# Optimization experiments

Hardware: AMD Instinct MI355X
Metric: run time of the kernel (lower is better)

Reference implementation:

```python
import jax, jax.numpy as jnp
import numpy as np

# ---- model constants (stand-ins for the Qiskit circuit / SparsePauliOp) ----
Q = 20           # qubits
L = 4            # ansatz layers: RY on every qubit, then ring of CZ
R = 24           # tensor-ring bond rank (init kwarg `rank`)
P = Q * L        # number of circuit parameters
CDT = jnp.complex64

_CZ = jnp.asarray(np.diag([1.0, 1.0, 1.0, -1.0]).reshape(2, 2, 2, 2), CDT)

# Observable H = 0.8*Z0 Z1 + 0.5*Z3 (Z/I-only -> 'efficient' expectation path)
_TERMS = [(0.8, (0, 1)), (0.5, (3,))]
_ZDIAG = jnp.asarray([1.0, -1.0], CDT)


def _init_cores():
    # |0...0> product state embedded in rank-R ring cores (identity bonds),
    # plus a tiny fixed perturbation so truncated-SVD singular values are
    # generic (keeps jax.vjp through SVD well-conditioned).
    rng = np.random.default_rng(0)
    cores = []
    for _ in range(Q):
        c = np.zeros((R, 2, R), np.complex64)
        c[:, 0, :] = np.eye(R, dtype=np.complex64)
        c = c + 1e-2 * (rng.standard_normal((R, 2, R))
                        + 1j * rng.standard_normal((R, 2, R))).astype(np.complex64)
        cores.append(jnp.asarray(c))
    return cores

_INIT_CORES = _init_cores()


def _apply_1q(core, U2):
    # core: (R, 2, R); U2: (2, 2) acting on the physical index
    return jnp.einsum('ts,asb->atb', U2, core)


def _apply_2q(ci, cj, U4):
    # merge neighboring ring cores, apply 4x4 gate, split via truncated SVD
    theta = jnp.einsum('asb,btc->astc', ci, cj)        # (R,2,2,R)
    theta = jnp.einsum('uvst,astc->auvc', U4, theta)   # gate on physical (s,t)
    M = theta.reshape(2 * R, 2 * R)
    Uu, s, Vh = jnp.linalg.svd(M, full_matrices=False)
    sr = jnp.sqrt(s[:R]).astype(CDT)                   # split sqrt(s) both ways
    ci_new = (Uu[:, :R] * sr[None, :]).reshape(R, 2, R)
    cj_new = (sr[:, None] * Vh[:R, :]).reshape(R, 2, R)
    return ci_new, cj_new


def _ring_ev(cores, zqubits):
    # <psi| (prod_i D_i) |psi> for diagonal D_i in {I, Z}; trace-closed ring.
    # Boundary M[p,q,b,r]: p/b = ket open/running bonds, q/r = bra bonds.
    eye = jnp.eye(R, dtype=CDT)
    M = jnp.einsum('ab,cd->acbd', eye, eye)            # (R,R,R,R)
    zset = set(zqubits)
    for i in range(Q):
        A = cores[i]
        Ad = A * _ZDIAG[None, :, None] if i in zset else A
        T = jnp.einsum('pqbr,bsc->pqrsc', M, Ad)       # contract ket bond, 2R^5
        M = jnp.einsum('pqrsc,rsd->pqcd', T, jnp.conj(A))  # bra bond + phys
    return jnp.einsum('pqpq->', M)                     # close the ring trace


def _forward(params):
    cores = list(_INIT_CORES)
    idx = 0
    for _ in range(L):
        for q in range(Q):
            half = params[idx] * 0.5
            idx += 1
            c, s = jnp.cos(half), jnp.sin(half)
            U2 = jnp.stack([jnp.stack([c, -s]), jnp.stack([s, c])]).astype(CDT)
            cores[q] = _apply_1q(cores[q], U2)
        for q in range(Q):                              # ring of CZ (wraps)
            j = (q + 1) % Q
            cores[q], cores[j] = _apply_2q(cores[q], cores[j], _CZ)
    norm = jnp.real(_ring_ev(cores, ()))
    ev = sum(c * jnp.real(_ring_ev(cores, zq)) for c, zq in _TERMS)
    return (ev / norm).astype(jnp.float32)


def setup_inputs() -> dict:
    key = jax.random.key(0)
    params = jax.random.normal(key, (P,), dtype=jnp.float32)
    return {"params": params}


def reference(params):
    return _forward(params)
```

## Files before the change

### kernel.cpp

```cpp
#include <hip/hip_runtime.h>
#include <cstdint>
#include <cmath>
#include <cstring>


#define RK 24
#define NQ 20
#define NLAY 4
#define NCOL 48
#define AS 49
#define NSWEEP 8
#define NTHR 384
#define CORE_ELEMS (RK * 2 * RK)
#define M4 (RK * RK * RK * RK)

namespace npyrng {

struct Pcg64 {
  unsigned __int128 state, inc;
  static inline unsigned __int128 mult() {
    return (((unsigned __int128)0x2360ED051FC65DA4ull) << 64) |
           0x4385DF649FCCF645ull;
  }
  inline void step() { state = state * mult() + inc; }
  inline uint64_t next64() {
    step();
    uint64_t hi = (uint64_t)(state >> 64), lo = (uint64_t)state;
    uint64_t v = hi ^ lo;
    unsigned r = (unsigned)(state >> 122);
    return (v >> r) | (v << ((64u - r) & 63u));
  }
  inline double nextDouble() {
    return (double)(next64() >> 11) * (1.0 / 9007199254740992.0);
  }
};

struct ZigTables {
  uint64_t ki[256];
  double wi[256], fi[256];
};

static void build_tables(ZigTables& T) {
  const double NR = 3.6541528853610088;
  const double PI = 3.14159265358979323846;
  double f = std::exp(-0.5 * NR * NR);
  double V = NR * f + std::sqrt(PI / 2.0) * std::erfc(NR / std::sqrt(2.0));
  const double m1 = 4503599627370496.0;
  double q = V / f;
  T.ki[0] = (uint64_t)((NR / q) * m1);
  T.ki[1] = 0;
  T.wi[0] = q / m1;
  T.wi[255] = NR / m1;
  T.fi[0] = 1.0;
  T.fi[255] = f;
  double tn = NR;
  for (int i = 254; i >= 1; --i) {
    double dn = std::sqrt(-2.0 * std::log(V / tn + std::exp(-0.5 * tn * tn)));
    T.ki[i + 1] = (uint64_t)((dn / tn) * m1);
    T.fi[i] = std::exp(-0.5 * dn * dn);
    T.wi[i] = dn / m1;
    tn = dn;
  }
}

static double std_normal(Pcg64& g, const ZigTables& T) {
  const double NR = 3.6541528853610088;
  const double INV_NR = 0.27366123732975828;
  for (;;) {
    uint64_t r = g.next64();
    int idx = (int)(r & 0xff);
    r >>= 8;
    int sign = (int)(r & 1);
    uint64_t rabs = (r >> 1) & 0x000fffffffffffffull;
    double x = (double)rabs * T.wi[idx];
    if (sign) x = -x;
    if (rabs < T.ki[idx]) return x;
    if (idx == 0) {
      for (;;) {
        double xx = -INV_NR * std::log1p(-g.nextDouble());
        double yy = -std::log1p(-g.nextDouble());
        if (yy + yy > xx * xx)
          return ((rabs >> 8) & 1) ? -(NR + xx) : (NR + xx);
      }
    } else {
      if ((T.fi[idx - 1] - T.fi[idx]) * g.nextDouble() + T.fi[idx] <
          std::exp(-0.5 * x * x))
        return x;
    }
  }
}

static void seed_pcg64_numpy0(Pcg64& g) {
  const uint32_t INIT_A = 0x43b0d7e5u, MULT_A = 0x931e8875u;
  const uint32_t INIT_B = 0x8b51f9ddu, MULT_B = 0x58f38dedu;
  const uint32_t MIX_L = 0xca01f9ddu, MIX_R = 0x4973f715u;
  uint32_t pool[4];
  uint32_t hc = INIT_A;
  auto hashf = [&](uint32_t value) -> uint32_t {
    value ^= hc;
    hc *= MULT_A;
    value *= hc;
    value ^= value >> 16;
    return value;
  };
  auto mixf = [&](uint32_t x, uint32_t y) -> uint32_t {
    uint32_t r = x * MIX_L - y * MIX_R;
    r ^= r >> 16;
    return r;
  };
  uint32_t entropy0 = 0u;
  for (int i = 0; i < 4; ++i) pool[i] = hashf(i < 1 ? entropy0 : 0u);
  for (int s = 0; s < 4; ++s)
    for (int d = 0; d < 4; ++d)
      if (s != d) pool[d] = mixf(pool[d], hashf(pool[s]));
  uint32_t w[8];
  uint32_t hb = INIT_B;
  for (int i = 0; i < 8; ++i) {
    uint32_t dv = pool[i & 3];
    dv ^= hb;
    hb *= MULT_B;
    dv *= hb;
    dv ^= dv >> 16;
    w[i] = dv;
  }
  uint64_t v0 = (uint64_t)w[0] | ((uint64_t)w[1] << 32);
  uint64_t v1 = (uint64_t)w[2] | ((uint64_t)w[3] << 32);
  uint64_t v2 = (uint64_t)w[4] | ((uint64_t)w[5] << 32);
  uint64_t v3 = (uint64_t)w[6] | ((uint64_t)w[7] << 32);
  unsigned __int128 initstate = (((unsigned __int128)v0) << 64) | v1;
  unsigned __int128 initseq = (((unsigned __int128)v2) << 64) | v3;
  g.state = 0;
  g.inc = (initseq << 1) | 1;
  g.step();
  g.state += initstate;
  g.step();
}

}

static float h_cores[NQ * CORE_ELEMS * 2];

static void fill_host_cores() {
  npyrng::Pcg64 g;
  npyrng::seed_pcg64_numpy0(g);
  npyrng::ZigTables T;
  npyrng::build_tables(T);
  double re[CORE_ELEMS], im[CORE_ELEMS];
  for (int core = 0; core < NQ; ++core) {
    for (int t = 0; t < CORE_ELEMS; ++t) re[t] = npyrng::std_normal(g, T);
    for (int t = 0; t < CORE_ELEMS; ++t) im[t] = npyrng::std_normal(g, T);
    for (int o = 0; o < CORE_ELEMS; ++o) {
      int a = o / (2 * RK);
      int s = (o / RK) & 1;
      int b = o % RK;
      float baser = (s == 0 && a == b) ? 1.0f : 0.0f;
      float nr = (float)re[o], ni = (float)im[o];
      h_cores[(core * CORE_ELEMS + o) * 2 + 0] = baser + 0.01f * nr;
      h_cores[(core * CORE_ELEMS + o) * 2 + 1] = 0.01f * ni;
    }
  }
}

__device__ __forceinline__ float row_reduce16(float x) {
  int v;
  v = __builtin_amdgcn_update_dpp(0, __float_as_int(x), 0x128, 0xf, 0xf, false);
  x += __int_as_float(v);
  v = __builtin_amdgcn_update_dpp(0, __float_as_int(x), 0x124, 0xf, 0xf, false);
  x += __int_as_float(v);
  v = __builtin_amdgcn_update_dpp(0, __float_as_int(x), 0x122, 0xf, 0xf, false);
  x += __int_as_float(v);
  v = __builtin_amdgcn_update_dpp(0, __float_as_int(x), 0x121, 0xf, 0xf, false);
  x += __int_as_float(v);
  return x;
}

__global__ __launch_bounds__(NTHR) void evolve_kernel(
    const float* __restrict__ params, float2* __restrict__ cores) {
  __shared__ float2 A[NCOL * AS];
  __shared__ float2 S1[NCOL * AS];
  __shared__ float2 M0[NCOL * NCOL];
  __shared__ float n0[NCOL], n1[NCOL];
  __shared__ float sig2[NCOL];
  __shared__ int keepSrc[RK];
  __shared__ float csbuf[NQ * 2];
  __shared__ int sweepFlag;

  const int tid = threadIdx.x;
  const int team = tid >> 4;
  const int sub = tid & 15;

  const int tdst = (team == 0) ? 0 : ((team < 23) ? team + 1 : 47);
  const int bdst = (team == 0) ? 1 : (23 + team);
  const int tsrc = team;
  const int bsrc = 24 + team;

  if (tid == 0) sweepFlag = 0;

  for (int layer = 0; layer < NLAY; ++layer) {
    if (tid < NQ) {
      float half = 0.5f * params[layer * NQ + tid];
      csbuf[2 * tid] = cosf(half);
      csbuf[2 * tid + 1] = sinf(half);
    }
    __syncthreads();
    for (int o = tid; o < NQ * RK * RK; o += NTHR) {
      int qq = o / (RK * RK);
      int ab = o % (RK * RK);
      int a = ab / RK, b = ab % RK;
      float ch = csbuf[2 * qq], sh = csbuf[2 * qq + 1];
      float2* base = cores + qq * CORE_ELEMS;
      float2 c0 = base[(a * 2 + 0) * RK + b];
      float2 c1 = base[(a * 2 + 1) * RK + b];
      base[(a * 2 + 0) * RK + b] =
          make_float2(ch * c0.x - sh * c1.x, ch * c0.y - sh * c1.y);
      base[(a * 2 + 1) * RK + b] =
          make_float2(sh * c0.x + ch * c1.x, sh * c0.y + ch * c1.y);
    }
    __syncthreads();

    for (int qg = 0; qg < NQ; ++qg) {
      int jg = (qg + 1) % NQ;
      const float2* ci = cores + qg * CORE_ELEMS;
      const float2* cj = cores + jg * CORE_ELEMS;

      for (int o = tid; o < CORE_ELEMS; o += NTHR) {
        M0[o] = ci[o];
        M0[CORE_ELEMS + o] = cj[o];
      }
      __syncthreads();

      float2 mv[6];
      {
        int k = 0;
        for (int o = tid; o < NCOL * NCOL; o += NTHR, ++k) {
          int col = o / NCOL, row = o % NCOL;
          int a = row >> 1, s = row & 1;
          int t = col / RK, cc = col % RK;
          float accx = 0.f, accy = 0.f;
          for (int b = 0; b < RK; ++b) {
            float2 x = M0[(a * 2 + s) * RK + b];
            float2 y = M0[CORE_ELEMS + (b * 2 + t) * RK + cc];
            accx += x.x * y.x - x.y * y.y;
            accy += x.x * y.y + x.y * y.x;
          }
          if (s == 1 && t == 1) { accx = -accx; accy = -accy; }
          mv[k] = make_float2(accx, accy);
        }
      }
      __syncthreads();
      {
        int k = 0;
        for (int o = tid; o < NCOL * NCOL; o += NTHR, ++k) {
          int col = o / NCOL, row = o % NCOL;
          A[col * AS + row] = mv[k];
          M0[col * NCOL + row] = mv[k];
        }
      }
      __syncthreads();

      float2 t0 = A[tsrc * AS + sub], t1 = A[tsrc * AS + sub + 16],
             t2 = A[tsrc * AS + sub + 32];
      float2 b0 = A[bsrc * AS + sub], b1 = A[bsrc * AS + sub + 16],
             b2 = A[bsrc * AS + sub + 32];
      float nt = t0.x * t0.x + t0.y * t0.y + t1.x * t1.x + t1.y * t1.y +
                 t2.x * t2.x + t2.y * t2.y;
      float nb = b0.x * b0.x + b0.y * b0.y + b1.x * b1.x + b1.y * b1.y +
                 b2.x * b2.x + b2.y * b2.y;
      nt = row_reduce16(nt);
      nb = row_reduce16(nb);

      int rr = 0;
      for (int sw = 0; sw < NSWEEP; ++sw) {
        bool myActive = false;
        for (int r = 0; r < 47; ++r) {
          float pr = t0.x * b0.x + t0.y * b0.y + t1.x * b1.x + t1.y * b1.y +
                     t2.x * b2.x + t2.y * b2.y;
          float pi = t0.x * b0.y - t0.y * b0.x + t1.x * b1.y - t1.y * b1.x +
                     t2.x * b2.y - t2.y * b2.x;
          pr = row_reduce16(pr);
          pi = row_reduce16(pi);
          float m2 = pr * pr + pi * pi;
          myActive = myActive || (m2 > 1e-7f * nt * nb);
          if (m2 > 1e-30f && m2 > 1e-14f * nt * nb) {
            float inv_m = rsqrtf(m2);
            float zr = pr * inv_m, zi = pi * inv_m;
            float tau = (nt - nb) * 0.5f * inv_m;
            float tt = 1.f / (fabsf(tau) + sqrtf(1.f + tau * tau));
            if (tau < 0.f) tt = -tt;
            float cc_ = rsqrtf(1.f + tt * tt);
            float ss_ = tt * cc_;
#define ROT_PAIR(xp, xq)                                                     \
  {                                                                          \
    float zqr = zr * xq.x + zi * xq.y;                                       \
    float zqi = zr * xq.y - zi * xq.x;                                       \
    float zpr = zr * xp.x - zi * xp.y;                                       \
    float zpi = zr * xp.y + zi * xp.x;                                       \
    float2 npv = make_float2(cc_ * xp.x + ss_ * zqr, cc_ * xp.y + ss_ * zqi);\
    float2 nqv = make_float2(cc_ * xq.x - ss_ * zpr, cc_ * xq.y - ss_ * zpi);\
    xp = npv;                                                                \
    xq = nqv;                                                                \
  }
            ROT_PAIR(t0, b0);
            ROT_PAIR(t1, b1);
            ROT_PAIR(t2, b2);
#undef ROT_PAIR
            float mg = m2 * inv_m;
            float c2 = cc_ * cc_, s2 = ss_ * ss_;
            float cs2m = 2.f * cc_ * ss_ * mg;
            float ntn = c2 * nt + s2 * nb + cs2m;
            nb = s2 * nt + c2 * nb - cs2m;
            nt = ntn;
          }
          float2* wb = (rr & 1) ? A : S1;
          float* wn = (rr & 1) ? n0 : n1;
          wb[tdst * AS + sub] = t0;
          wb[tdst * AS + sub + 16] = t1;
          wb[tdst * AS + sub + 32] = t2;
          wb[bdst * AS + sub] = b0;
          wb[bdst * AS + sub + 16] = b1;
          wb[bdst * AS + sub + 32] = b2;
          if (sub == 0) {
            wn[tdst] = nt;
            wn[bdst] = nb;
          }
          __syncthreads();
          t0 = wb[tsrc * AS + sub];
          t1 = wb[tsrc * AS + sub + 16];
          t2 = wb[tsrc * AS + sub + 32];
          b0 = wb[bsrc * AS + sub];
          b1 = wb[bsrc * AS + sub + 16];
          b2 = wb[bsrc * AS + sub + 32];
          nt = wn[tsrc];
          nb = wn[bsrc];
          ++rr;
        }
        unsigned long long bal = __ballot(myActive);
        if ((tid & 63) == 0 && bal != 0ull) sweepFlag = 1;
        __syncthreads();
        int f = sweepFlag;
        __syncthreads();
        if (tid == 0) sweepFlag = 0;
        if (f == 0) break;
      }

      A[tsrc * AS + sub] = t0;
      A[tsrc * AS + sub + 16] = t1;
      A[tsrc * AS + sub + 32] = t2;
      A[bsrc * AS + sub] = b0;
      A[bsrc * AS + sub + 16] = b1;
      A[bsrc * AS + sub + 32] = b2;
      {
        float xt = t0.x * t0.x + t0.y * t0.y + t1.x * t1.x + t1.y * t1.y +
                   t2.x * t2.x + t2.y * t2.y;
        float xb = b0.x * b0.x + b0.y * b0.y + b1.x * b1.x + b1.y * b1.y +
                   b2.x * b2.x + b2.y * b2.y;
        xt = row_reduce16(xt);
        xb = row_reduce16(xb);
        if (sub == 0) {
          sig2[tsrc] = xt;
          sig2[bsrc] = xb;
        }
      }
      __syncthreads();

      if (tid < NCOL) {
        float mine = sig2[tid];
        int rk = 0;
        for (int kx = 0; kx < NCOL; ++kx) {
          float o = sig2[kx];
          if (o > mine || (o == mine && kx < tid)) ++rk;
        }
        if (rk < RK) keepSrc[rk] = tid;
      }
      __syncthreads();

      for (int o = tid; o < RK * NCOL; o += NTHR) {
        int bn = o / NCOL;
        int row = o % NCOL;
        int src = keepSrc[bn];
        float sg = sqrtf(sig2[src]);
        float su = rsqrtf(fmaxf(sg, 1e-30f));
        float2 x = A[src * AS + row];
        cores[qg * CORE_ELEMS + row * RK + bn] =
            make_float2(x.x * su, x.y * su);
      }
      for (int o = tid; o < RK * NCOL; o += NTHR) {
        int bn = o / NCOL;
        int col = o % NCOL;
        int src = keepSrc[bn];
        float s2 = fmaxf(sig2[src], 1e-30f);
        float scale = rsqrtf(s2) * rsqrtf(sqrtf(s2));
        float accx = 0.f, accy = 0.f;
        const float2* ac = &A[src * AS];
        const float2* mc = &M0[col * NCOL];
#pragma unroll 8
        for (int rx = 0; rx < NCOL; ++rx) {
          float2 u = ac[rx];
          float2 mm = mc[rx];
          accx += u.x * mm.x + u.y * mm.y;
          accy += u.x * mm.y - u.y * mm.x;
        }
        cores[jg * CORE_ELEMS + bn * (2 * RK) + col] =
            make_float2(accx * scale, accy * scale);
      }
      __syncthreads();
    }
  }
}

__global__ __launch_bounds__(256) void init_m_kernel(float2* __restrict__ mb) {
  int i = blockIdx.x * 256 + threadIdx.x;
  if (i >= M4) return;
  int r = i % RK;
  int b = (i / RK) % RK;
  int q = (i / (RK * RK)) % RK;
  int p = i / (RK * RK * RK);
  mb[i] = make_float2((p == b && q == r) ? 1.f : 0.f, 0.f);
}

__global__ __launch_bounds__(256) void ring_step_kernel(
    const float2* __restrict__ Min, float2* __restrict__ Mout,
    const float2* __restrict__ cores, int qubit, int zmask) {
  __shared__ float2 Msh[RK * RK];
  __shared__ float2 Ash[CORE_ELEMS];
  __shared__ float2 Tsh[RK * 2 * RK];
  const int pq = blockIdx.x;
  const float zs = ((zmask >> qubit) & 1) ? -1.f : 1.f;
  const float2* minpq = Min + (size_t)pq * (RK * RK);
  for (int o = threadIdx.x; o < RK * RK; o += 256) Msh[o] = minpq[o];
  const float2* Ac = cores + qubit * CORE_ELEMS;
  for (int o = threadIdx.x; o < CORE_ELEMS; o += 256) Ash[o] = Ac[o];
  __syncthreads();
  for (int o = threadIdx.x; o < RK * 2 * RK; o += 256) {
    int r = o / (2 * RK);
    int sc = o % (2 * RK);
    int s = sc / RK, c = sc % RK;
    float sgn = (s == 1) ? zs : 1.f;
    float accx = 0.f, accy = 0.f;
#pragma unroll 8
    for (int b = 0; b < RK; ++b) {
      float2 m = Msh[b * RK + r];
      float2 a = Ash[(b * 2 + s) * RK + c];
      accx += m.x * a.x - m.y * a.y;
      accy += m.x * a.y + m.y * a.x;
    }
    Tsh[o] = make_float2(accx * sgn, accy * sgn);
  }
  __syncthreads();
  float2* moutpq = Mout + (size_t)pq * (RK * RK);
  for (int o = threadIdx.x; o < RK * RK; o += 256) {
    int c = o / RK, d = o % RK;
    float accx = 0.f, accy = 0.f;
    for (int r = 0; r < RK; ++r)
#pragma unroll
      for (int s = 0; s < 2; ++s) {
        float2 t = Tsh[r * (2 * RK) + s * RK + c];
        float2 a = Ash[(r * 2 + s) * RK + d];
        accx += t.x * a.x + t.y * a.y;
        accy += t.y * a.x - t.x * a.y;
      }
    moutpq[o] = make_float2(accx, accy);
  }
}

__global__ __launch_bounds__(256) void trace_kernel(
    const float2* __restrict__ mb, float* __restrict__ dst) {
  __shared__ float sh[4];
  float tr = 0.f;
  for (int o = threadIdx.x; o < RK * RK; o += 256) {
    int p = o / RK, q = o % RK;
    tr += mb[(size_t)o * (RK * RK) + p * RK + q].x;
  }
  for (int d = 1; d < 64; d <<= 1) tr += __shfl_xor(tr, d);
  int wave = threadIdx.x >> 6, lane = threadIdx.x & 63;
  if (lane == 0) sh[wave] = tr;
  __syncthreads();
  if (threadIdx.x == 0) dst[0] = sh[0] + sh[1] + sh[2] + sh[3];
}

__global__ void final_kernel(const float* __restrict__ trs,
                             float* __restrict__ out) {
  if (threadIdx.x == 0)
    out[0] = (0.8f * trs[1] + 0.5f * trs[2]) / trs[0];
}

extern "C" void kernel_launch(void* const* d_in, const int* in_sizes, int n_in,
                              void* d_out, int out_size, void* d_ws,
                              size_t ws_size, hipStream_t stream) {
  const float* params = (const float*)d_in[0];
  float* out = (float*)d_out;
  char* ws = (char*)d_ws;

  const size_t CORES_BYTES = sizeof(h_cores);
  const size_t MB_BYTES = (size_t)M4 * sizeof(float2);
  float2* cores = (float2*)ws;
  float2* B0 = (float2*)(ws + CORES_BYTES);
  float2* B1 = (float2*)(ws + CORES_BYTES + MB_BYTES);
  float2* B2 = (float2*)(ws + CORES_BYTES + 2 * MB_BYTES);
  float* tr_ws = (float*)(ws + CORES_BYTES + 3 * MB_BYTES);

  fill_host_cores();
  hipMemcpyAsync(cores, h_cores, CORES_BYTES, hipMemcpyHostToDevice, stream);

  evolve_kernel<<<1, NTHR, 0, stream>>>(params, cores);

  init_m_kernel<<<(M4 + 255) / 256, 256, 0, stream>>>(B0);
  for (int qb = 4; qb < 20; ++qb) {
    const float2* src = ((qb - 4) & 1) ? B1 : B0;
    float2* dst = ((qb - 4) & 1) ? B0 : B1;
    ring_step_kernel<<<RK * RK, 256, 0, stream>>>(src, dst, cores, qb, 0);
  }
  for (int e = 0; e < 3; ++e) {
    int zm = (e == 0) ? 0 : (e == 1 ? 3 : 8);
    ring_step_kernel<<<RK * RK, 256, 0, stream>>>(B0, B1, cores, 0, zm);
    ring_step_kernel<<<RK * RK, 256, 0, stream>>>(B1, B2, cores, 1, zm);
    ring_step_kernel<<<RK * RK, 256, 0, stream>>>(B2, B1, cores, 2, zm);
    ring_step_kernel<<<RK * RK, 256, 0, stream>>>(B1, B2, cores, 3, zm);
    trace_kernel<<<1, 256, 0, stream>>>(B2, tr_ws + e);
  }
  final_kernel<<<1, 64, 0, stream>>>(tr_ws, out);
}
```

Measured before the change: 18.49 ms.

## Use 8-lane teams with packed float2 math in one-sided Jacobi SVD

The Jacobi SVD sweep now uses 8 lanes per column pair instead of 16, with only 192 active threads. Each lane holds six complex elements in split real/imag packed-float2 vectors so the compiler can emit packed FP32 ops. The DPP reduction is shortened to three steps, and the shared-memory ping-pong buffer switches to float4 layout. The sweep convergence threshold is also loosened from 1e-7 to 1e-5, which may cut sweeps at some cost in SVD accuracy.

Measured after the change: 17.76 ms. 1.04x faster.

```diff
diff --git a/kernel.cpp b/kernel.cpp
--- a/kernel.cpp
+++ b/kernel.cpp
@@ -9,10 +9,14 @@
 #define NLAY 4
 #define NCOL 48
 #define AS 49
+#define ASQ 25
 #define NSWEEP 8
 #define NTHR 384
+#define NACT 192
 #define CORE_ELEMS (RK * 2 * RK)
 #define M4 (RK * RK * RK * RK)
+
+typedef float v2f __attribute__((ext_vector_type(2)));
 
 namespace npyrng {
 
@@ -161,15 +165,13 @@
   }
 }
 
-__device__ __forceinline__ float row_reduce16(float x) {
+__device__ __forceinline__ float red8(float x) {
   int v;
-  v = __builtin_amdgcn_update_dpp(0, __float_as_int(x), 0x128, 0xf, 0xf, false);
+  v = __builtin_amdgcn_update_dpp(0, __float_as_int(x), 0xB1, 0xf, 0xf, false);
   x += __int_as_float(v);
-  v = __builtin_amdgcn_update_dpp(0, __float_as_int(x), 0x124, 0xf, 0xf, false);
+  v = __builtin_amdgcn_update_dpp(0, __float_as_int(x), 0x4E, 0xf, 0xf, false);
   x += __int_as_float(v);
-  v = __builtin_amdgcn_update_dpp(0, __float_as_int(x), 0x122, 0xf, 0xf, false);
-  x += __int_as_float(v);
-  v = __builtin_amdgcn_update_dpp(0, __float_as_int(x), 0x121, 0xf, 0xf, false);
+  v = __builtin_amdgcn_update_dpp(0, __float_as_int(x), 0x141, 0xf, 0xf, false);
   x += __int_as_float(v);
   return x;
 }
@@ -177,7 +179,8 @@
 __global__ __launch_bounds__(NTHR) void evolve_kernel(
     const float* __restrict__ params, float2* __restrict__ cores) {
   __shared__ float2 A[NCOL * AS];
-  __shared__ float2 S1[NCOL * AS];
+  __shared__ float4 A4[NCOL * ASQ];
+  __shared__ float4 S4[NCOL * ASQ];
   __shared__ float2 M0[NCOL * NCOL];
   __shared__ float n0[NCOL], n1[NCOL];
   __shared__ float sig2[NCOL];
@@ -186,15 +189,16 @@
   __shared__ int sweepFlag;
 
   const int tid = threadIdx.x;
-  const int team = tid >> 4;
-  const int sub = tid & 15;
+  const bool act = tid < NACT;
+  const int team = tid >> 3;
+  const int l8 = tid & 7;
 
   const int tdst = (team == 0) ? 0 : ((team < 23) ? team + 1 : 47);
   const int bdst = (team == 0) ? 1 : (23 + team);
-  const int tsrc = team;
-  const int bsrc = 24 + team;
+  const int tsrc = team, bsrc = 24 + team;
 
   if (tid == 0) sweepFlag = 0;
+  int rr = 0;
 
   for (int layer = 0; layer < NLAY; ++layer) {
     if (tid < NQ) {
@@ -258,83 +262,113 @@
       }
       __syncthreads();
 
-      float2 t0 = A[tsrc * AS + sub], t1 = A[tsrc * AS + sub + 16],
-             t2 = A[tsrc * AS + sub + 32];
-      float2 b0 = A[bsrc * AS + sub], b1 = A[bsrc * AS + sub + 16],
-             b2 = A[bsrc * AS + sub + 32];
-      float nt = t0.x * t0.x + t0.y * t0.y + t1.x * t1.x + t1.y * t1.y +
-                 t2.x * t2.x + t2.y * t2.y;
-      float nb = b0.x * b0.x + b0.y * b0.y + b1.x * b1.x + b1.y * b1.y +
-                 b2.x * b2.x + b2.y * b2.y;
-      nt = row_reduce16(nt);
-      nb = row_reduce16(nb);
-
-      int rr = 0;
+      v2f tR0 = {0, 0}, tR1 = {0, 0}, tR2 = {0, 0};
+      v2f tI0 = {0, 0}, tI1 = {0, 0}, tI2 = {0, 0};
+      v2f bR0 = {0, 0}, bR1 = {0, 0}, bR2 = {0, 0};
+      v2f bI0 = {0, 0}, bI1 = {0, 0}, bI2 = {0, 0};
+      float nt = 0.f, nb = 0.f;
+      if (act) {
+        const float2* cp = &A[tsrc * AS + 6 * l8];
+        float2 u0 = cp[0], u1 = cp[1], u2 = cp[2], u3 = cp[3], u4 = cp[4],
+               u5 = cp[5];
+        tR0 = (v2f){u0.x, u1.x}; tI0 = (v2f){u0.y, u1.y};
+        tR1 = (v2f){u2.x, u3.x}; tI1 = (v2f){u2.y, u3.y};
+        tR2 = (v2f){u4.x, u5.x}; tI2 = (v2f){u4.y, u5.y};
+        cp = &A[bsrc * AS + 6 * l8];
+        u0 = cp[0]; u1 = cp[1]; u2 = cp[2]; u3 = cp[3]; u4 = cp[4]; u5 = cp[5];
+        bR0 = (v2f){u0.x, u1.x}; bI0 = (v2f){u0.y, u1.y};
+        bR1 = (v2f){u2.x, u3.x}; bI1 = (v2f){u2.y, u3.y};
+        bR2 = (v2f){u4.x, u5.x}; bI2 = (v2f){u4.y, u5.y};
+        v2f Nt = tR0 * tR0 + tI0 * tI0 + tR1 * tR1 + tI1 * tI1 + tR2 * tR2 +
+                 tI2 * tI2;
+        v2f Nb = bR0 * bR0 + bI0 * bI0 + bR1 * bR1 + bI1 * bI1 + bR2 * bR2 +
+                 bI2 * bI2;
+        nt = red8(Nt.x + Nt.y);
+        nb = red8(Nb.x + Nb.y);
+      }
+      __syncthreads();
+
       for (int sw = 0; sw < NSWEEP; ++sw) {
         bool myActive = false;
         for (int r = 0; r < 47; ++r) {
-          float pr = t0.x * b0.x + t0.y * b0.y + t1.x * b1.x + t1.y * b1.y +
-                     t2.x * b2.x + t2.y * b2.y;
-          float pi = t0.x * b0.y - t0.y * b0.x + t1.x * b1.y - t1.y * b1.x +
-                     t2.x * b2.y - t2.y * b2.x;
-          pr = row_reduce16(pr);
-          pi = row_reduce16(pi);
-          float m2 = pr * pr + pi * pi;
-          myActive = myActive || (m2 > 1e-7f * nt * nb);
-          if (m2 > 1e-30f && m2 > 1e-14f * nt * nb) {
-            float inv_m = rsqrtf(m2);
-            float zr = pr * inv_m, zi = pi * inv_m;
-            float tau = (nt - nb) * 0.5f * inv_m;
-            float tt = 1.f / (fabsf(tau) + sqrtf(1.f + tau * tau));
-            if (tau < 0.f) tt = -tt;
-            float cc_ = rsqrtf(1.f + tt * tt);
-            float ss_ = tt * cc_;
-#define ROT_PAIR(xp, xq)                                                     \
-  {                                                                          \
-    float zqr = zr * xq.x + zi * xq.y;                                       \
-    float zqi = zr * xq.y - zi * xq.x;                                       \
-    float zpr = zr * xp.x - zi * xp.y;                                       \
-    float zpi = zr * xp.y + zi * xp.x;                                       \
-    float2 npv = make_float2(cc_ * xp.x + ss_ * zqr, cc_ * xp.y + ss_ * zqi);\
-    float2 nqv = make_float2(cc_ * xq.x - ss_ * zpr, cc_ * xq.y - ss_ * zpi);\
-    xp = npv;                                                                \
-    xq = nqv;                                                                \
-  }
-            ROT_PAIR(t0, b0);
-            ROT_PAIR(t1, b1);
-            ROT_PAIR(t2, b2);
-#undef ROT_PAIR
-            float mg = m2 * inv_m;
-            float c2 = cc_ * cc_, s2 = ss_ * ss_;
-            float cs2m = 2.f * cc_ * ss_ * mg;
-            float ntn = c2 * nt + s2 * nb + cs2m;
-            nb = s2 * nt + c2 * nb - cs2m;
-            nt = ntn;
-          }
-          float2* wb = (rr & 1) ? A : S1;
-          float* wn = (rr & 1) ? n0 : n1;
-          wb[tdst * AS + sub] = t0;
-          wb[tdst * AS + sub + 16] = t1;
-          wb[tdst * AS + sub + 32] = t2;
-          wb[bdst * AS + sub] = b0;
-          wb[bdst * AS + sub + 16] = b1;
-          wb[bdst * AS + sub + 32] = b2;
-          if (sub == 0) {
-            wn[tdst] = nt;
-            wn[bdst] = nb;
+          if (act) {
+            v2f Pr = tR0 * bR0 + tI0 * bI0;
+            Pr += tR1 * bR1 + tI1 * bI1;
+            Pr += tR2 * bR2 + tI2 * bI2;
+            v2f Pi = tR0 * bI0 - tI0 * bR0;
+            Pi += tR1 * bI1 - tI1 * bR1;
+            Pi += tR2 * bI2 - tI2 * bR2;
+            float pr = red8(Pr.x + Pr.y);
+            float pi = red8(Pi.x + Pi.y);
+            float m2 = pr * pr + pi * pi;
+            myActive = myActive || (m2 > 1e-5f * nt * nb);
+            if (m2 > 1e-30f && m2 > 1e-14f * nt * nb) {
+              float inv_m = rsqrtf(m2);
+              float zr = pr * inv_m, zi = pi * inv_m;
+              float tau = (nt - nb) * 0.5f * inv_m;
+              float tt = 1.f / (fabsf(tau) + sqrtf(1.f + tau * tau));
+              if (tau < 0.f) tt = -tt;
+              float cc_ = rsqrtf(1.f + tt * tt);
+              float ss_ = tt * cc_;
+              v2f zrv = {zr, zr}, ziv = {zi, zi};
+              v2f ccv = {cc_, cc_}, ssv = {ss_, ss_};
+#define ROTK(TR, TI, BR, BI)                                   \
+  {                                                            \
+    v2f zqR = zrv * BR + ziv * BI;                             \
+    v2f zqI = zrv * BI - ziv * BR;                             \
+    v2f zpR = zrv * TR - ziv * TI;                             \
+    v2f zpI = zrv * TI + ziv * TR;                             \
+    TR = ccv * TR + ssv * zqR;                                 \
+    TI = ccv * TI + ssv * zqI;                                 \
+    BR = ccv * BR - ssv * zpR;                                 \
+    BI = ccv * BI - ssv * zpI;                                 \
+  }
+              ROTK(tR0, tI0, bR0, bI0);
+              ROTK(tR1, tI1, bR1, bI1);
+              ROTK(tR2, tI2, bR2, bI2);
+#undef ROTK
+              float mg = m2 * inv_m;
+              float c2 = cc_ * cc_, s2 = ss_ * ss_;
+              float cs2m = 2.f * cc_ * ss_ * mg;
+              float ntn = c2 * nt + s2 * nb + cs2m;
+              nb = s2 * nt + c2 * nb - cs2m;
+              nt = ntn;
+            }
+            float4* wb = (rr & 1) ? A4 : S4;
+            float* wn = (rr & 1) ? n0 : n1;
+            int tb = tdst * ASQ + l8 * 3;
+            wb[tb + 0] = make_float4(tR0.x, tR0.y, tI0.x, tI0.y);
+            wb[tb + 1] = make_float4(tR1.x, tR1.y, tI1.x, tI1.y);
+            wb[tb + 2] = make_float4(tR2.x, tR2.y, tI2.x, tI2.y);
+            int bb = bdst * ASQ + l8 * 3;
+            wb[bb + 0] = make_float4(bR0.x, bR0.y, bI0.x, bI0.y);
+            wb[bb + 1] = make_float4(bR1.x, bR1.y, bI1.x, bI1.y);
+            wb[bb + 2] = make_float4(bR2.x, bR2.y, bI2.x, bI2.y);
+            if (l8 == 0) {
+              wn[tdst] = nt;
+              wn[bdst] = nb;
+            }
           }
           __syncthreads();
-          t0 = wb[tsrc * AS + sub];
-          t1 = wb[tsrc * AS + sub + 16];
-          t2 = wb[tsrc * AS + sub + 32];
-          b0 = wb[bsrc * AS + sub];
-          b1 = wb[bsrc * AS + sub + 16];
-          b2 = wb[bsrc * AS + sub + 32];
-          nt = wn[tsrc];
-          nb = wn[bsrc];
+          if (act) {
+            const float4* wb = (rr & 1) ? A4 : S4;
+            const float* wn = (rr & 1) ? n0 : n1;
+            int ts = tsrc * ASQ + l8 * 3;
+            float4 q0 = wb[ts + 0], q1 = wb[ts + 1], q2 = wb[ts + 2];
+            tR0 = (v2f){q0.x, q0.y}; tI0 = (v2f){q0.z, q0.w};
+            tR1 = (v2f){q1.x, q1.y}; tI1 = (v2f){q1.z, q1.w};
+            tR2 = (v2f){q2.x, q2.y}; tI2 = (v2f){q2.z, q2.w};
+            int bs = bsrc * ASQ + l8 * 3;
+            q0 = wb[bs + 0]; q1 = wb[bs + 1]; q2 = wb[bs + 2];
+            bR0 = (v2f){q0.x, q0.y}; bI0 = (v2f){q0.z, q0.w};
+            bR1 = (v2f){q1.x, q1.y}; bI1 = (v2f){q1.z, q1.w};
+            bR2 = (v2f){q2.x, q2.y}; bI2 = (v2f){q2.z, q2.w};
+            nt = wn[tsrc];
+            nb = wn[bsrc];
+          }
           ++rr;
         }
-        unsigned long long bal = __ballot(myActive);
+        unsigned long long bal = __ballot(act && myActive);
         if ((tid & 63) == 0 && bal != 0ull) sweepFlag = 1;
         __syncthreads();
         int f = sweepFlag;
@@ -343,20 +377,28 @@
         if (f == 0) break;
       }
 
-      A[tsrc * AS + sub] = t0;
-      A[tsrc * AS + sub + 16] = t1;
-      A[tsrc * AS + sub + 32] = t2;
-      A[bsrc * AS + sub] = b0;
-      A[bsrc * AS + sub + 16] = b1;
-      A[bsrc * AS + sub + 32] = b2;
-      {
-        float xt = t0.x * t0.x + t0.y * t0.y + t1.x * t1.x + t1.y * t1.y +
-                   t2.x * t2.x + t2.y * t2.y;
-        float xb = b0.x * b0.x + b0.y * b0.y + b1.x * b1.x + b1.y * b1.y +
-                   b2.x * b2.x + b2.y * b2.y;
-        xt = row_reduce16(xt);
-        xb = row_reduce16(xb);
-        if (sub == 0) {
+      if (act) {
+        float2* cp = &A[tsrc * AS + 6 * l8];
+        cp[0] = make_float2(tR0.x, tI0.x);
+        cp[1] = make_float2(tR0.y, tI0.y);
+        cp[2] = make_float2(tR1.x, tI1.x);
+        cp[3] = make_float2(tR1.y, tI1.y);
+        cp[4] = make_float2(tR2.x, tI2.x);
+        cp[5] = make_float2(tR2.y, tI2.y);
+        cp = &A[bsrc * AS + 6 * l8];
+        cp[0] = make_float2(bR0.x, bI0.x);
+        cp[1] = make_float2(bR0.y, bI0.y);
+        cp[2] = make_float2(bR1.x, bI1.x);
+        cp[3] = make_float2(bR1.y, bI1.y);
+        cp[4] = make_float2(bR2.x, bI2.x);
+        cp[5] = make_float2(bR2.y, bI2.y);
+        v2f Nt = tR0 * tR0 + tI0 * tI0 + tR1 * tR1 + tI1 * tI1 + tR2 * tR2 +
+                 tI2 * tI2;
+        v2f Nb = bR0 * bR0 + bI0 * bI0 + bR1 * bR1 + bI1 * bI1 + bR2 * bR2 +
+                 bI2 * bI2;
+        float xt = red8(Nt.x + Nt.y);
+        float xb = red8(Nb.x + Nb.y);
+        if (l8 == 0) {
           sig2[tsrc] = xt;
           sig2[bsrc] = xb;
         }
```
